# Kernel tuning notes

Hardware: AMD Instinct MI355X
Metric: run time of the kernel (lower is better)

Reference implementation:

```python
import jax, jax.numpy as jnp
import numpy as np

DIM = 512
HEADS = 8
HEAD_DIM = DIM // HEADS
LN_EPS = 1e-5


def setup_inputs() -> dict:
    key = jax.random.key(0)
    ks = jax.random.split(key, 16)
    B, L, E = 4, 4096, DIM
    x = jax.random.normal(ks[0], (B, L, E), dtype=jnp.float32)
    w = lambda k: jax.random.normal(k, (E, E), dtype=jnp.float32) * 0.02
    b = lambda k: jax.random.normal(k, (E,), dtype=jnp.float32) * 0.02
    return {
        "x": x,
        "ln_gamma": jnp.ones((E,), jnp.float32),
        "ln_beta": jnp.zeros((E,), jnp.float32),
        "Wqr": w(ks[1]), "bqr": b(ks[2]),
        "Wqi": w(ks[3]), "bqi": b(ks[4]),
        "Wkr": w(ks[5]), "bkr": b(ks[6]),
        "Wki": w(ks[7]), "bki": b(ks[8]),
        "Wvr": w(ks[9]), "bvr": b(ks[10]),
        "Wvi": w(ks[11]), "bvi": b(ks[12]),
        "Wo": w(ks[13]),
    }


def reference(x, ln_gamma, ln_beta, Wqr, bqr, Wqi, bqi, Wkr, bkr, Wki, bki,
              Wvr, bvr, Wvi, bvi, Wo):
    B, L, E = x.shape
    H, d = HEADS, HEAD_DIM
    # LayerNorm over last dim
    mu = jnp.mean(x, axis=-1, keepdims=True)
    var = jnp.mean(jnp.square(x - mu), axis=-1, keepdims=True)
    xn = (x - mu) * jax.lax.rsqrt(var + LN_EPS) * ln_gamma + ln_beta
    # rfft along time dim -> F = L//2 + 1 frequency bins
    xf = jnp.fft.rfft(xn, axis=1, norm="ortho")
    xr, xi = jnp.real(xf), jnp.imag(xf)  # [B, F, E]
    # split real/imag QKV projections (torch Linear: y = x @ W.T + b)
    Qr = xr @ Wqr.T + bqr
    Qi = xi @ Wqi.T + bqi
    Kr = xr @ Wkr.T + bkr
    Ki = xi @ Wki.T + bki
    Vr = xr @ Wvr.T + bvr
    Vi = xi @ Wvi.T + bvi
    Fn = xr.shape[1]
    split = lambda t: t.reshape(B, Fn, H, d)  # b l (h d) -> b l h d
    Qr, Qi, Kr, Ki, Vr, Vi = map(split, (Qr, Qi, Kr, Ki, Vr, Vi))
    # scores = Qr.Kr + Qi.Ki, scaled softmax over keys
    scores = (jnp.einsum("blhd,bmhd->bhlm", Qr, Kr)
              + jnp.einsum("blhd,bmhd->bhlm", Qi, Ki))
    attn = jax.nn.softmax(scores * (d ** -0.5), axis=-1)
    out_r = jnp.einsum("bhlm,bmhd->bhld", attn, Vr)
    out_i = jnp.einsum("bhlm,bmhd->bhld", attn, Vi)
    out_f = jax.lax.complex(out_r, out_i)  # [B, H, F, d]
    out_f = jnp.transpose(out_f, (0, 2, 1, 3)).reshape(B, Fn, E)
    out_t = jnp.fft.irfft(out_f, n=L, axis=1, norm="ortho")
    return out_t @ Wo.T
```

## Files before the change

### kernel.cpp

```cpp
#include <hip/hip_runtime.h>
#include <math.h>

#define NB 4
#define NL 4096
#define NE 512
#define NH 8
#define ND 64
#define NF 2049
#define WSZ (NE * NE)

static constexpr float INV_SQRT_N = 1.0f / 64.0f;

typedef __attribute__((ext_vector_type(8))) short bf16x8;
typedef __attribute__((ext_vector_type(4))) short short4v;
typedef __attribute__((ext_vector_type(4))) float f32x4;

__device__ __forceinline__ float2 cmul(float2 a, float2 b) {
    return make_float2(a.x * b.x - a.y * b.y, a.x * b.y + a.y * b.x);
}

__device__ __forceinline__ short cvt_bf16(float f) {
    unsigned u = __float_as_uint(f);
    unsigned r = (u + 0x7FFFu + ((u >> 16) & 1u)) >> 16;
    return (short)r;
}

__device__ __forceinline__ int pack_bf16x2(float a, float b) {
    return (int)(unsigned short)cvt_bf16(a) | ((int)(unsigned short)cvt_bf16(b) << 16);
}

__device__ __forceinline__ float2 unpk(int v) {
    return make_float2(__uint_as_float(((unsigned)v & 0xffffu) << 16),
                       __uint_as_float((unsigned)v & 0xffff0000u));
}

__device__ __forceinline__ int b4rev(int t) {
    int r = __brev((unsigned)t) >> 20;
    return ((r & 0x555) << 1) | ((r & 0xAAA) >> 1);
}

__global__ __launch_bounds__(256) void twiddle_kernel(float2* __restrict__ twg) {
    int j = blockIdx.x * 256 + threadIdx.x;
    double ang = (2.0 * M_PI / (double)NL) * (double)j;
    double s, c;
    sincos(ang, &s, &c);
    twg[j] = make_float2((float)c, (float)s);
}

__global__ __launch_bounds__(256) void castw_kernel(
    const float* __restrict__ w0, const float* __restrict__ w1,
    const float* __restrict__ w2, const float* __restrict__ w3,
    const float* __restrict__ w4, const float* __restrict__ w5,
    const float* __restrict__ w6, short* __restrict__ dst) {
    int which = blockIdx.y;
    const float* s = which == 0 ? w0 : which == 1 ? w1 : which == 2 ? w2 :
                     which == 3 ? w3 : which == 4 ? w4 : which == 5 ? w5 : w6;
    long i = (long)blockIdx.x * 1024 + threadIdx.x * 4;
    float4 v = *(const float4*)(s + i);
    short4v o = {cvt_bf16(v.x), cvt_bf16(v.y), cvt_bf16(v.z), cvt_bf16(v.w)};
    *(short4v*)(dst + (long)which * WSZ + i) = o;
}

__global__ __launch_bounds__(256) void ln_kernel(
    const float* __restrict__ x, const float* __restrict__ g,
    const float* __restrict__ be, short* __restrict__ xnb) {
    int wv = threadIdx.x >> 6, lane = threadIdx.x & 63;
    long row = (long)blockIdx.x * 4 + wv;
    const float* xp = x + row * NE + lane * 8;
    float4 a = *(const float4*)xp;
    float4 b = *(const float4*)(xp + 4);
    float s  = a.x + a.y + a.z + a.w + b.x + b.y + b.z + b.w;
    float ss = a.x * a.x + a.y * a.y + a.z * a.z + a.w * a.w
             + b.x * b.x + b.y * b.y + b.z * b.z + b.w * b.w;
#pragma unroll
    for (int o = 32; o; o >>= 1) { s += __shfl_xor(s, o); ss += __shfl_xor(ss, o); }
    float mu = s * (1.0f / NE);
    float var = ss * (1.0f / NE) - mu * mu;
    float rs = rsqrtf(var + 1e-5f);
    const float* gp = g + lane * 8;
    const float* bp = be + lane * 8;
    float4 g0 = *(const float4*)gp, g1 = *(const float4*)(gp + 4);
    float4 b0 = *(const float4*)bp, b1 = *(const float4*)(bp + 4);
    bf16x8 ov;
    ov[0] = cvt_bf16((a.x - mu) * rs * g0.x + b0.x);
    ov[1] = cvt_bf16((a.y - mu) * rs * g0.y + b0.y);
    ov[2] = cvt_bf16((a.z - mu) * rs * g0.z + b0.z);
    ov[3] = cvt_bf16((a.w - mu) * rs * g0.w + b0.w);
    ov[4] = cvt_bf16((b.x - mu) * rs * g1.x + b1.x);
    ov[5] = cvt_bf16((b.y - mu) * rs * g1.y + b1.y);
    ov[6] = cvt_bf16((b.z - mu) * rs * g1.z + b1.z);
    ov[7] = cvt_bf16((b.w - mu) * rs * g1.w + b1.w);
    *(bf16x8*)(xnb + row * NE + lane * 8) = ov;
}

template <int INV>
__device__ __forceinline__ void fft4_stages(float2* sdata, const float2* tws, int tid) {
#pragma unroll
    for (int st = 0; st < 6; ++st) {
        __syncthreads();
        int Q = 1 << (2 * st);
        int tq = 10 - 2 * st;
#pragma unroll
        for (int jj = 0; jj < 4; ++jj) {
            int j = tid + jj * 256;
            int k = j & (Q - 1);
            int i0 = ((j >> (2 * st)) << (2 * st + 2)) | k;
            float2 w1 = tws[k << tq];
            float2 w2 = tws[(2 * k) << tq];
            float2 w3 = cmul(w1, w2);
            float2 a = sdata[i0];
            float2 b = cmul(w1, sdata[i0 + Q]);
            float2 c = cmul(w2, sdata[i0 + 2 * Q]);
            float2 d = cmul(w3, sdata[i0 + 3 * Q]);
            float2 t0 = make_float2(a.x + c.x, a.y + c.y);
            float2 t1 = make_float2(a.x - c.x, a.y - c.y);
            float2 t2 = make_float2(b.x + d.x, b.y + d.y);
            float2 bd = make_float2(b.x - d.x, b.y - d.y);
            float2 t3 = INV ? make_float2(-bd.y, bd.x) : make_float2(bd.y, -bd.x);
            sdata[i0]         = make_float2(t0.x + t2.x, t0.y + t2.y);
            sdata[i0 + Q]     = make_float2(t1.x + t3.x, t1.y + t3.y);
            sdata[i0 + 2 * Q] = make_float2(t0.x - t2.x, t0.y - t2.y);
            sdata[i0 + 3 * Q] = make_float2(t1.x - t3.x, t1.y - t3.y);
        }
    }
    __syncthreads();
}

__device__ __forceinline__ int ep_swizzle(int loc) {
    return ((loc & 7) << 5) | (loc >> 3);
}

__global__ __launch_bounds__(256) void rfft_pair(
    const short* __restrict__ xnb, const float2* __restrict__ twg,
    short* __restrict__ xr, short* __restrict__ xi) {
    __shared__ float2 sdata[NL];
    __shared__ float2 tws[NL / 2];
    int b = blockIdx.x >> 8;
    int e0 = ep_swizzle(blockIdx.x & 255) * 2;
    int tid = threadIdx.x;
    const short* xp = xnb + (long)b * NL * NE + e0;
#pragma unroll
    for (int jj = 0; jj < 16; ++jj) {
        int t = tid + jj * 256;
        int v = *(const int*)(xp + (long)t * NE);
        sdata[b4rev(t)] = unpk(v);
    }
#pragma unroll
    for (int jj = 0; jj < 8; ++jj) {
        int j = tid + jj * 256;
        float2 w = twg[j];
        tws[j] = make_float2(w.x, -w.y);
    }
    fft4_stages<0>(sdata, tws, tid);
    short* xrp = xr + (long)b * NF * NE + e0;
    short* xip = xi + (long)b * NF * NE + e0;
    for (int f = tid; f < NF; f += 256) {
        int M = (NL - f) & (NL - 1);
        float2 zf = sdata[f], zm = sdata[M];
        float re0 = (zf.x + zm.x) * (0.5f * INV_SQRT_N);
        float im0 = (zf.y - zm.y) * (0.5f * INV_SQRT_N);
        float re1 = (zf.y + zm.y) * (0.5f * INV_SQRT_N);
        float im1 = (zm.x - zf.x) * (0.5f * INV_SQRT_N);
        *(int*)(xrp + (long)f * NE) = pack_bf16x2(re0, re1);
        *(int*)(xip + (long)f * NE) = pack_bf16x2(im0, im1);
    }
}

__global__ __launch_bounds__(256) void irfft_pair(
    const short* __restrict__ orr, const short* __restrict__ oii,
    const float2* __restrict__ twg, short* __restrict__ yt) {
    __shared__ float2 sdata[NL];
    __shared__ float2 tws[NL / 2];
    int b = blockIdx.x >> 8;
    int e0 = ep_swizzle(blockIdx.x & 255) * 2;
    int tid = threadIdx.x;
    const short* orp = orr + (long)b * NF * NE + e0;
    const short* oip = oii + (long)b * NF * NE + e0;
    for (int f = tid; f < NF; f += 256) {
        float2 vr = unpk(*(const int*)(orp + (long)f * NE));
        float2 vi = unpk(*(const int*)(oip + (long)f * NE));
        if (f == 0 || f == NL / 2) vi = make_float2(0.f, 0.f);
        sdata[b4rev(f)] = make_float2(vr.x - vi.y, vi.x + vr.y);
        if (f > 0 && f < NL / 2) {
            sdata[b4rev(NL - f)] = make_float2(vr.x + vi.y, vr.y - vi.x);
        }
    }
#pragma unroll
    for (int jj = 0; jj < 8; ++jj) {
        int j = tid + jj * 256;
        tws[j] = twg[j];
    }
    fft4_stages<1>(sdata, tws, tid);
    short* yp = yt + (long)b * NL * NE + e0;
#pragma unroll
    for (int jj = 0; jj < 16; ++jj) {
        int t = tid + jj * 256;
        float2 z = sdata[t];
        *(int*)(yp + (long)t * NE) = pack_bf16x2(z.x * INV_SQRT_N, z.y * INV_SQRT_N);
    }
}

__device__ __forceinline__ void gemm_core(
    const short* __restrict__ A, const short* __restrict__ W,
    const float* __restrict__ bias, float scale, short* __restrict__ Cb,
    float* __restrict__ Cf, int N) {
    __shared__ short As[128][40];
    __shared__ short Bs[128][40];
    int o0 = blockIdx.x * 128;
    int n0 = blockIdx.y * 128;
    int tid = threadIdx.x;
    int lane = tid & 63, wv = tid >> 6;
    int quad = lane >> 4, cl = lane & 15;
    int rbase = (wv >> 1) << 6;
    int cbase = (wv & 1) << 6;
    int srow = tid >> 2;
    int sseg = tid & 3;
    f32x4 acc[4][4];
#pragma unroll
    for (int i = 0; i < 4; ++i)
#pragma unroll
        for (int j = 0; j < 4; ++j) acc[i][j] = (f32x4){0, 0, 0, 0};

    int ra = n0 + srow;      if (ra >= N) ra = N - 1;
    int rb = n0 + srow + 64; if (rb >= N) rb = N - 1;
    const short* Ap0 = A + (long)ra * NE + sseg * 8;
    const short* Ap1 = A + (long)rb * NE + sseg * 8;
    const short* Wp0 = W + (long)(o0 + srow) * NE + sseg * 8;
    const short* Wp1 = W + (long)(o0 + srow + 64) * NE + sseg * 8;

    bf16x8 a0 = *(const bf16x8*)Ap0, a1 = *(const bf16x8*)Ap1;
    bf16x8 b0 = *(const bf16x8*)Wp0, b1 = *(const bf16x8*)Wp1;

    for (int kt = 0; kt < 16; ++kt) {
        __syncthreads();
        *(bf16x8*)&As[srow][sseg * 8] = a0;
        *(bf16x8*)&As[srow + 64][sseg * 8] = a1;
        *(bf16x8*)&Bs[srow][sseg * 8] = b0;
        *(bf16x8*)&Bs[srow + 64][sseg * 8] = b1;
        __syncthreads();
        if (kt < 15) {
            int ko = (kt + 1) * 32;
            a0 = *(const bf16x8*)(Ap0 + ko);
            a1 = *(const bf16x8*)(Ap1 + ko);
            b0 = *(const bf16x8*)(Wp0 + ko);
            b1 = *(const bf16x8*)(Wp1 + ko);
        }
        bf16x8 ar[4], br[4];
#pragma unroll
        for (int i = 0; i < 4; ++i) ar[i] = *(const bf16x8*)&As[rbase + 16 * i + cl][quad * 8];
#pragma unroll
        for (int j = 0; j < 4; ++j) br[j] = *(const bf16x8*)&Bs[cbase + 16 * j + cl][quad * 8];
#pragma unroll
        for (int i = 0; i < 4; ++i)
#pragma unroll
            for (int j = 0; j < 4; ++j)
                acc[i][j] = __builtin_amdgcn_mfma_f32_16x16x32_bf16(ar[i], br[j], acc[i][j], 0, 0, 0);
    }
    float bv[4];
#pragma unroll
    for (int j = 0; j < 4; ++j) bv[j] = bias ? bias[o0 + cbase + 16 * j + cl] : 0.0f;
#pragma unroll
    for (int i = 0; i < 4; ++i) {
#pragma unroll
        for (int r = 0; r < 4; ++r) {
            int n = n0 + rbase + 16 * i + quad * 4 + r;
            if (n >= N) continue;
#pragma unroll
            for (int j = 0; j < 4; ++j) {
                float v = (acc[i][j][r] + bv[j]) * scale;
                int o = o0 + cbase + 16 * j + cl;
                if (Cb) Cb[(long)n * NE + o] = cvt_bf16(v);
                else    Cf[(long)n * NE + o] = v;
            }
        }
    }
}

__global__ __launch_bounds__(256) void gemm_qkv(
    const short* __restrict__ A,
    const short* __restrict__ W0, const short* __restrict__ W1, const short* __restrict__ W2,
    const float* __restrict__ b0, const float* __restrict__ b1, const float* __restrict__ b2,
    short* __restrict__ C0, short* __restrict__ C1, short* __restrict__ C2, int N) {
    int z = blockIdx.z;
    const short* W = z == 0 ? W0 : z == 1 ? W1 : W2;
    const float* bb = z == 0 ? b0 : z == 1 ? b1 : b2;
    short* C = z == 0 ? C0 : z == 1 ? C1 : C2;
    gemm_core(A, W, bb, z == 0 ? 0.125f : 1.0f, C, nullptr, N);
}

__global__ __launch_bounds__(256) void gemm_out(
    const short* __restrict__ A, const short* __restrict__ W,
    float* __restrict__ C, int N) {
    gemm_core(A, W, nullptr, 1.0f, nullptr, C, N);
}

__global__ __launch_bounds__(256) void fattn_mfma(
    const short* __restrict__ Qr, const short* __restrict__ Qi,
    const short* __restrict__ Kr, const short* __restrict__ Ki,
    const short* __restrict__ Vr, const short* __restrict__ Vi,
    short* __restrict__ Orb, short* __restrict__ Oib) {
    __shared__ short Ks[2][64][72];
    __shared__ short Vt[2][64][72];
    int tid = threadIdx.x;
    int wv = tid >> 6, lane = tid & 63;
    int quad = lane >> 4, cl = lane & 15;
    int h = blockIdx.y, b = blockIdx.z;
    long base = (long)b * NF * NE + h * ND;
    int qbase = blockIdx.x * 64 + wv * 16;

    int sk0 = (tid >> 4) << 2;
    int sd0 = (tid & 15) << 2;
    int g0 = tid >> 4;
    int dsw = tid & 15;

    bf16x8 qar[2], qai[2];
    {
        int qrow = qbase + cl; if (qrow >= NF) qrow = NF - 1;
        const short* pr = Qr + base + (long)qrow * NE + 8 * quad;
        const short* pi = Qi + base + (long)qrow * NE + 8 * quad;
        qar[0] = *(const bf16x8*)pr;
        qar[1] = *(const bf16x8*)(pr + 32);
        qai[0] = *(const bf16x8*)pi;
        qai[1] = *(const bf16x8*)(pi + 32);
    }

    float ls = 0.f;
    f32x4 Or2[4], Oi2[4];
#pragma unroll
    for (int t = 0; t < 4; ++t) { Or2[t] = (f32x4){0,0,0,0}; Oi2[t] = (f32x4){0,0,0,0}; }

    short4v lk0[4], lk1[4], lv0[4], lv1[4];
    auto ldtile = [&](int m0) {
        short4v z4 = {0, 0, 0, 0};
#pragma unroll
        for (int kk = 0; kk < 4; ++kk) {
            int mg = m0 + sk0 + kk;
            if (mg < NF) {
                long roff = base + (long)mg * NE + sd0;
                lk0[kk] = *(const short4v*)(Kr + roff);
                lk1[kk] = *(const short4v*)(Ki + roff);
                lv0[kk] = *(const short4v*)(Vr + roff);
                lv1[kk] = *(const short4v*)(Vi + roff);
            } else { lk0[kk] = z4; lk1[kk] = z4; lv0[kk] = z4; lv1[kk] = z4; }
        }
    };
    ldtile(0);

    for (int kt = 0; kt < 33; ++kt) {
        int m0 = kt * 64;
        __syncthreads();
#pragma unroll
        for (int kk = 0; kk < 4; ++kk) {
            *(short4v*)&Ks[0][sk0 + kk][sd0] = lk0[kk];
            *(short4v*)&Ks[1][sk0 + kk][sd0] = lk1[kk];
        }
        {
            int cv = (g0 ^ dsw) << 2;
#pragma unroll
            for (int dd = 0; dd < 4; ++dd) {
                short4v t0 = {lv0[0][dd], lv0[1][dd], lv0[2][dd], lv0[3][dd]};
                *(short4v*)&Vt[0][sd0 + dd][cv] = t0;
                short4v t1 = {lv1[0][dd], lv1[1][dd], lv1[2][dd], lv1[3][dd]};
                *(short4v*)&Vt[1][sd0 + dd][cv] = t1;
            }
        }
        __syncthreads();
        if (kt + 1 < 33) ldtile(m0 + 64);

        f32x4 c[4];
#pragma unroll
        for (int t = 0; t < 4; ++t) {
            f32x4 acc = (f32x4){0, 0, 0, 0};
            const short* kr = &Ks[0][cl + 16 * t][8 * quad];
            const short* ki = &Ks[1][cl + 16 * t][8 * quad];
            acc = __builtin_amdgcn_mfma_f32_16x16x32_bf16(*(const bf16x8*)kr, qar[0], acc, 0, 0, 0);
            acc = __builtin_amdgcn_mfma_f32_16x16x32_bf16(*(const bf16x8*)(kr + 32), qar[1], acc, 0, 0, 0);
            acc = __builtin_amdgcn_mfma_f32_16x16x32_bf16(*(const bf16x8*)ki, qai[0], acc, 0, 0, 0);
            acc = __builtin_amdgcn_mfma_f32_16x16x32_bf16(*(const bf16x8*)(ki + 32), qai[1], acc, 0, 0, 0);
            c[t] = acc;
        }

        short4v pb[4];
#pragma unroll
        for (int t = 0; t < 4; ++t) {
            int kbase = m0 + 16 * t + quad * 4;
#pragma unroll
            for (int r = 0; r < 4; ++r) {
                float p = (kbase + r < NF) ? __expf(c[t][r]) : 0.0f;
                c[t][r] = p;
                ls += p;
            }
            pb[t] = (short4v){cvt_bf16(c[t][0]), cvt_bf16(c[t][1]),
                              cvt_bf16(c[t][2]), cvt_bf16(c[t][3])};
        }

#pragma unroll
        for (int nt = 0; nt < 4; ++nt) {
            int d = cl + 16 * nt;
            int dg = (d >> 2) & 15;
#pragma unroll
            for (int t = 0; t < 4; ++t) {
                int g = 4 * t + quad;
                int cv = ((g ^ dg) << 2);
                short4v va = *(const short4v*)&Vt[0][d][cv];
                short4v vb = *(const short4v*)&Vt[1][d][cv];
                Or2[nt] = __builtin_amdgcn_mfma_f32_16x16x16bf16_1k(va, pb[t], Or2[nt], 0, 0, 0);
                Oi2[nt] = __builtin_amdgcn_mfma_f32_16x16x16bf16_1k(vb, pb[t], Oi2[nt], 0, 0, 0);
            }
        }
    }

    ls += __shfl_xor(ls, 16);
    ls += __shfl_xor(ls, 32);
    float inv = 1.0f / ls;
    int q = qbase + cl;
    if (q < NF) {
        short* po = Orb + base + (long)q * NE;
        short* pi2 = Oib + base + (long)q * NE;
#pragma unroll
        for (int nt = 0; nt < 4; ++nt) {
            int d0 = 16 * nt + quad * 4;
            short4v so = {cvt_bf16(Or2[nt][0] * inv), cvt_bf16(Or2[nt][1] * inv),
                          cvt_bf16(Or2[nt][2] * inv), cvt_bf16(Or2[nt][3] * inv)};
            *(short4v*)(po + d0) = so;
            short4v si = {cvt_bf16(Oi2[nt][0] * inv), cvt_bf16(Oi2[nt][1] * inv),
                          cvt_bf16(Oi2[nt][2] * inv), cvt_bf16(Oi2[nt][3] * inv)};
            *(short4v*)(pi2 + d0) = si;
        }
    }
}

extern "C" void kernel_launch(void* const* d_in, const int* in_sizes, int n_in,
                              void* d_out, int out_size, void* d_ws, size_t ws_size,
                              hipStream_t stream) {
    const float* x   = (const float*)d_in[0];
    const float* g   = (const float*)d_in[1];
    const float* be  = (const float*)d_in[2];
    const float* Wqr = (const float*)d_in[3];
    const float* bqr = (const float*)d_in[4];
    const float* Wqi = (const float*)d_in[5];
    const float* bqi = (const float*)d_in[6];
    const float* Wkr = (const float*)d_in[7];
    const float* bkr = (const float*)d_in[8];
    const float* Wki = (const float*)d_in[9];
    const float* bki = (const float*)d_in[10];
    const float* Wvr = (const float*)d_in[11];
    const float* bvr = (const float*)d_in[12];
    const float* Wvi = (const float*)d_in[13];
    const float* bvi = (const float*)d_in[14];
    const float* Wo  = (const float*)d_in[15];
    float* out = (float*)d_out;

    const long SZ_T = (long)NB * NL * NE;
    const long SZ_F = (long)NB * NF * NE;
    float2* twg = (float2*)d_ws;
    short* xnb = (short*)(twg + 2048);
    short* xr  = xnb + SZ_T;
    short* xi  = xr + SZ_F;
    short* Qr  = xi + SZ_F;
    short* Qi  = Qr + SZ_F;
    short* Kr  = Qi + SZ_F;
    short* Ki  = Kr + SZ_F;
    short* Vr  = Ki + SZ_F;
    short* Vi  = Vr + SZ_F;
    short* Orb = Vi + SZ_F;
    short* Oib = Orb + SZ_F;
    short* yt  = Oib + SZ_F;
    short* wb  = yt + SZ_T;

    twiddle_kernel<<<NL / 2 / 256, 256, 0, stream>>>(twg);
    castw_kernel<<<dim3(WSZ / 1024, 7), 256, 0, stream>>>(Wqr, Wqi, Wkr, Wki, Wvr, Wvi, Wo, wb);
    ln_kernel<<<NB * NL / 4, 256, 0, stream>>>(x, g, be, xnb);
    rfft_pair<<<NB * 256, 256, 0, stream>>>(xnb, twg, xr, xi);
    int Nf = NB * NF;
    dim3 gq(NE / 128, (Nf + 127) / 128, 3);
    gemm_qkv<<<gq, 256, 0, stream>>>(xr, wb + 0L * WSZ, wb + 2L * WSZ, wb + 4L * WSZ,
                                     bqr, bkr, bvr, Qr, Kr, Vr, Nf);
    gemm_qkv<<<gq, 256, 0, stream>>>(xi, wb + 1L * WSZ, wb + 3L * WSZ, wb + 5L * WSZ,
                                     bqi, bki, bvi, Qi, Ki, Vi, Nf);
    fattn_mfma<<<dim3(33, NH, NB), 256, 0, stream>>>(Qr, Qi, Kr, Ki, Vr, Vi, Orb, Oib);
    irfft_pair<<<NB * 256, 256, 0, stream>>>(Orb, Oib, twg, yt);
    gemm_out<<<dim3(NE / 128, NB * NL / 128), 256, 0, stream>>>(yt, wb + 6L * WSZ, out, NB * NL);
}
```

Baseline: 445.1 us.

## Process two query tiles per wave in frequency attention to reuse K/V tiles

Each wave now handles 32 query rows (two 16-row sub-tiles), so each block covers 128 queries and the grid shrinks from 33 to 17 blocks along the query axis. Every K/V fragment read from shared memory feeds twice as many MFMAs, halving global K/V traffic and LDS reads per query. K/V loads also use incrementing pointers without bounds checks except on the last tile, softmax masking runs only on the final tile, and s_setprio is raised around MFMA sections. The cost is higher register pressure and fewer blocks (544), which may lower occupancy and leave CUs underfilled.

```diff
diff --git a/kernel.cpp b/kernel.cpp
--- a/kernel.cpp
+++ b/kernel.cpp
@@ -306,45 +306,68 @@
     int quad = lane >> 4, cl = lane & 15;
     int h = blockIdx.y, b = blockIdx.z;
     long base = (long)b * NF * NE + h * ND;
-    int qbase = blockIdx.x * 64 + wv * 16;
+    int qbase = blockIdx.x * 128 + wv * 32;
 
     int sk0 = (tid >> 4) << 2;
     int sd0 = (tid & 15) << 2;
     int g0 = tid >> 4;
     int dsw = tid & 15;
 
-    bf16x8 qar[2], qai[2];
-    {
-        int qrow = qbase + cl; if (qrow >= NF) qrow = NF - 1;
+    bf16x8 qar[2][2], qai[2][2];
+#pragma unroll
+    for (int u = 0; u < 2; ++u) {
+        int qrow = qbase + 16 * u + cl; if (qrow >= NF) qrow = NF - 1;
         const short* pr = Qr + base + (long)qrow * NE + 8 * quad;
         const short* pi = Qi + base + (long)qrow * NE + 8 * quad;
-        qar[0] = *(const bf16x8*)pr;
-        qar[1] = *(const bf16x8*)(pr + 32);
-        qai[0] = *(const bf16x8*)pi;
-        qai[1] = *(const bf16x8*)(pi + 32);
-    }
-
-    float ls = 0.f;
-    f32x4 Or2[4], Oi2[4];
-#pragma unroll
-    for (int t = 0; t < 4; ++t) { Or2[t] = (f32x4){0,0,0,0}; Oi2[t] = (f32x4){0,0,0,0}; }
+        qar[u][0] = *(const bf16x8*)pr;
+        qar[u][1] = *(const bf16x8*)(pr + 32);
+        qai[u][0] = *(const bf16x8*)pi;
+        qai[u][1] = *(const bf16x8*)(pi + 32);
+    }
+
+    float ls[2] = {0.f, 0.f};
+    f32x4 Or2[4][2], Oi2[4][2];
+#pragma unroll
+    for (int t = 0; t < 4; ++t)
+#pragma unroll
+        for (int u = 0; u < 2; ++u) {
+            Or2[t][u] = (f32x4){0, 0, 0, 0};
+            Oi2[t][u] = (f32x4){0, 0, 0, 0};
+        }
 
     short4v lk0[4], lk1[4], lv0[4], lv1[4];
-    auto ldtile = [&](int m0) {
+    const short* pKr = Kr + base + (long)sk0 * NE + sd0;
+    const short* pKi = Ki + base + (long)sk0 * NE + sd0;
+    const short* pVr = Vr + base + (long)sk0 * NE + sd0;
+    const short* pVi = Vi + base + (long)sk0 * NE + sd0;
+    const long TSTEP = (long)64 * NE;
+
+    auto ldfull = [&]() {
+#pragma unroll
+        for (int kk = 0; kk < 4; ++kk) {
+            long o = (long)kk * NE;
+            lk0[kk] = *(const short4v*)(pKr + o);
+            lk1[kk] = *(const short4v*)(pKi + o);
+            lv0[kk] = *(const short4v*)(pVr + o);
+            lv1[kk] = *(const short4v*)(pVi + o);
+        }
+        pKr += TSTEP; pKi += TSTEP; pVr += TSTEP; pVi += TSTEP;
+    };
+    auto ldmask = [&](int m0) {
         short4v z4 = {0, 0, 0, 0};
 #pragma unroll
         for (int kk = 0; kk < 4; ++kk) {
             int mg = m0 + sk0 + kk;
             if (mg < NF) {
-                long roff = base + (long)mg * NE + sd0;
-                lk0[kk] = *(const short4v*)(Kr + roff);
-                lk1[kk] = *(const short4v*)(Ki + roff);
-                lv0[kk] = *(const short4v*)(Vr + roff);
-                lv1[kk] = *(const short4v*)(Vi + roff);
+                long o = (long)kk * NE;
+                lk0[kk] = *(const short4v*)(pKr + o);
+                lk1[kk] = *(const short4v*)(pKi + o);
+                lv0[kk] = *(const short4v*)(pVr + o);
+                lv1[kk] = *(const short4v*)(pVi + o);
             } else { lk0[kk] = z4; lk1[kk] = z4; lv0[kk] = z4; lv1[kk] = z4; }
         }
     };
-    ldtile(0);
+    ldfull();
 
     for (int kt = 0; kt < 33; ++kt) {
         int m0 = kt * 64;
@@ -365,35 +388,63 @@
             }
         }
         __syncthreads();
-        if (kt + 1 < 33) ldtile(m0 + 64);
-
-        f32x4 c[4];
+        if (kt < 31) ldfull();
+        else if (kt == 31) ldmask(m0 + 64);
+
+        f32x4 c[4][2];
+        __builtin_amdgcn_s_setprio(1);
 #pragma unroll
         for (int t = 0; t < 4; ++t) {
-            f32x4 acc = (f32x4){0, 0, 0, 0};
             const short* kr = &Ks[0][cl + 16 * t][8 * quad];
             const short* ki = &Ks[1][cl + 16 * t][8 * quad];
-            acc = __builtin_amdgcn_mfma_f32_16x16x32_bf16(*(const bf16x8*)kr, qar[0], acc, 0, 0, 0);
-            acc = __builtin_amdgcn_mfma_f32_16x16x32_bf16(*(const bf16x8*)(kr + 32), qar[1], acc, 0, 0, 0);
-            acc = __builtin_amdgcn_mfma_f32_16x16x32_bf16(*(const bf16x8*)ki, qai[0], acc, 0, 0, 0);
-            acc = __builtin_amdgcn_mfma_f32_16x16x32_bf16(*(const bf16x8*)(ki + 32), qai[1], acc, 0, 0, 0);
-            c[t] = acc;
-        }
-
-        short4v pb[4];
-#pragma unroll
-        for (int t = 0; t < 4; ++t) {
-            int kbase = m0 + 16 * t + quad * 4;
-#pragma unroll
-            for (int r = 0; r < 4; ++r) {
-                float p = (kbase + r < NF) ? __expf(c[t][r]) : 0.0f;
-                c[t][r] = p;
-                ls += p;
+            bf16x8 k0 = *(const bf16x8*)kr;
+            bf16x8 k1 = *(const bf16x8*)(kr + 32);
+            bf16x8 k2 = *(const bf16x8*)ki;
+            bf16x8 k3 = *(const bf16x8*)(ki + 32);
+#pragma unroll
+            for (int u = 0; u < 2; ++u) {
+                f32x4 acc = (f32x4){0, 0, 0, 0};
+                acc = __builtin_amdgcn_mfma_f32_16x16x32_bf16(k0, qar[u][0], acc, 0, 0, 0);
+                acc = __builtin_amdgcn_mfma_f32_16x16x32_bf16(k1, qar[u][1], acc, 0, 0, 0);
+                acc = __builtin_amdgcn_mfma_f32_16x16x32_bf16(k2, qai[u][0], acc, 0, 0, 0);
+                acc = __builtin_amdgcn_mfma_f32_16x16x32_bf16(k3, qai[u][1], acc, 0, 0, 0);
+                c[t][u] = acc;
             }
-            pb[t] = (short4v){cvt_bf16(c[t][0]), cvt_bf16(c[t][1]),
-                              cvt_bf16(c[t][2]), cvt_bf16(c[t][3])};
-        }
-
+        }
+        __builtin_amdgcn_s_setprio(0);
+
+        short4v pb[4][2];
+        if (kt < 32) {
+#pragma unroll
+            for (int t = 0; t < 4; ++t)
+#pragma unroll
+                for (int u = 0; u < 2; ++u) {
+                    float p0 = __expf(c[t][u][0]);
+                    float p1 = __expf(c[t][u][1]);
+                    float p2 = __expf(c[t][u][2]);
+                    float p3 = __expf(c[t][u][3]);
+                    ls[u] += (p0 + p1) + (p2 + p3);
+                    pb[t][u] = (short4v){cvt_bf16(p0), cvt_bf16(p1),
+                                         cvt_bf16(p2), cvt_bf16(p3)};
+                }
+        } else {
+#pragma unroll
+            for (int t = 0; t < 4; ++t) {
+                int kbase = m0 + 16 * t + quad * 4;
+#pragma unroll
+                for (int u = 0; u < 2; ++u) {
+                    float p0 = (kbase + 0 < NF) ? __expf(c[t][u][0]) : 0.0f;
+                    float p1 = (kbase + 1 < NF) ? __expf(c[t][u][1]) : 0.0f;
+                    float p2 = (kbase + 2 < NF) ? __expf(c[t][u][2]) : 0.0f;
+                    float p3 = (kbase + 3 < NF) ? __expf(c[t][u][3]) : 0.0f;
+                    ls[u] += (p0 + p1) + (p2 + p3);
+                    pb[t][u] = (short4v){cvt_bf16(p0), cvt_bf16(p1),
+                                         cvt_bf16(p2), cvt_bf16(p3)};
+                }
+            }
+        }
+
+        __builtin_amdgcn_s_setprio(1);
 #pragma unroll
         for (int nt = 0; nt < 4; ++nt) {
             int d = cl + 16 * nt;
@@ -404,28 +455,36 @@
                 int cv = ((g ^ dg) << 2);
                 short4v va = *(const short4v*)&Vt[0][d][cv];
                 short4v vb = *(const short4v*)&Vt[1][d][cv];
-                Or2[nt] = __builtin_amdgcn_mfma_f32_16x16x16bf16_1k(va, pb[t], Or2[nt], 0, 0, 0);
-                Oi2[nt] = __builtin_amdgcn_mfma_f32_16x16x16bf16_1k(vb, pb[t], Oi2[nt], 0, 0, 0);
+#pragma unroll
+                for (int u = 0; u < 2; ++u) {
+                    Or2[nt][u] = __builtin_amdgcn_mfma_f32_16x16x16bf16_1k(va, pb[t][u], Or2[nt][u], 0, 0, 0);
+                    Oi2[nt][u] = __builtin_amdgcn_mfma_f32_16x16x16bf16_1k(vb, pb[t][u], Oi2[nt][u], 0, 0, 0);
+                }
             }
         }
-    }
-
-    ls += __shfl_xor(ls, 16);
-    ls += __shfl_xor(ls, 32);
-    float inv = 1.0f / ls;
-    int q = qbase + cl;
-    if (q < NF) {
-        short* po = Orb + base + (long)q * NE;
-        short* pi2 = Oib + base + (long)q * NE;
-#pragma unroll
-        for (int nt = 0; nt < 4; ++nt) {
-            int d0 = 16 * nt + quad * 4;
-            short4v so = {cvt_bf16(Or2[nt][0] * inv), cvt_bf16(Or2[nt][1] * inv),
-                          cvt_bf16(Or2[nt][2] * inv), cvt_bf16(Or2[nt][3] * inv)};
-            *(short4v*)(po + d0) = so;
-            short4v si = {cvt_bf16(Oi2[nt][0] * inv), cvt_bf16(Oi2[nt][1] * inv),
-                          cvt_bf16(Oi2[nt][2] * inv), cvt_bf16(Oi2[nt][3] * inv)};
-            *(short4v*)(pi2 + d0) = si;
+        __builtin_amdgcn_s_setprio(0);
+    }
+
+#pragma unroll
+    for (int u = 0; u < 2; ++u) {
+        float l2 = ls[u];
+        l2 += __shfl_xor(l2, 16);
+        l2 += __shfl_xor(l2, 32);
+        float inv = 1.0f / l2;
+        int q = qbase + 16 * u + cl;
+        if (q < NF) {
+            short* po = Orb + base + (long)q * NE;
+            short* pi2 = Oib + base + (long)q * NE;
+#pragma unroll
+            for (int nt = 0; nt < 4; ++nt) {
+                int d0 = 16 * nt + quad * 4;
+                short4v so = {cvt_bf16(Or2[nt][u][0] * inv), cvt_bf16(Or2[nt][u][1] * inv),
+                              cvt_bf16(Or2[nt][u][2] * inv), cvt_bf16(Or2[nt][u][3] * inv)};
+                *(short4v*)(po + d0) = so;
+                short4v si = {cvt_bf16(Oi2[nt][u][0] * inv), cvt_bf16(Oi2[nt][u][1] * inv),
+                              cvt_bf16(Oi2[nt][u][2] * inv), cvt_bf16(Oi2[nt][u][3] * inv)};
+                *(short4v*)(pi2 + d0) = si;
+            }
         }
     }
 }
@@ -478,7 +537,7 @@
                                      bqr, bkr, bvr, Qr, Kr, Vr, Nf);
     gemm_qkv<<<gq, 256, 0, stream>>>(xi, wb + 1L * WSZ, wb + 3L * WSZ, wb + 5L * WSZ,
                                      bqi, bki, bvi, Qi, Ki, Vi, Nf);
-    fattn_mfma<<<dim3(33, NH, NB), 256, 0, stream>>>(Qr, Qi, Kr, Ki, Vr, Vi, Orb, Oib);
+    fattn_mfma<<<dim3(17, NH, NB), 256, 0, stream>>>(Qr, Qi, Kr, Ki, Vr, Vi, Orb, Oib);
     irfft_pair<<<NB * 256, 256, 0, stream>>>(Orb, Oib, twg, yt);
     gemm_out<<<dim3(NE / 128, NB * NL / 128), 256, 0, stream>>>(yt, wb + 6L * WSZ, out, NB * NL);
 }
```

After: 451.7 us. Within noise of the previous version (+1.5%).
